# Kernel optimization log

Measured on AMD Instinct MI355X. Metric: run time of the kernel, lower is better.

The kernel has to match this reference:

```python
import jax, jax.numpy as jnp
import numpy as np

BN_EPS = 1e-5


def fps(xyz, npoint):
    # farthest point sampling; xyz: (B,N,3) -> (B,npoint) int32, starts at index 0 (torch convention)
    B, N, _ = xyz.shape
    def step(carry, _):
        dist, last = carry
        lp = jnp.take_along_axis(xyz, last[:, None, None], axis=1)  # (B,1,3)
        d = jnp.sum((xyz - lp) ** 2, -1)                             # (B,N)
        dist = jnp.minimum(dist, d)
        nxt = jnp.argmax(dist, -1).astype(jnp.int32)
        return (dist, nxt), nxt
    init = (jnp.full((B, N), 1e10, xyz.dtype), jnp.zeros((B,), jnp.int32))
    _, rest = jax.lax.scan(step, init, None, length=npoint - 1)
    return jnp.concatenate([jnp.zeros((1, B), jnp.int32), rest], 0).T  # (B,npoint)


def knn_idx(xyz, centers, k):
    # xyz (B,N,3), centers (B,S,3) -> (B,S,k) nearest-neighbor indices
    d = (jnp.sum(centers ** 2, -1)[:, :, None]
         + jnp.sum(xyz ** 2, -1)[:, None, :]
         - 2.0 * jnp.einsum('bsc,bnc->bsn', centers, xyz))
    _, idx = jax.lax.top_k(-d, k)
    return idx


def group(feat, idx):
    # feat (B,N,C), idx (B,S,K) -> (B,S,K,C)
    return jax.vmap(lambda f, i: f[i])(feat, idx)


def sa_knn(xyz, points, npoint, nsample, w1, b1, w2, b2):
    # xyz (B,N,3), points (B,N,C); returns new_xyz (B,S,3), new_points (B,S,Cout)
    fidx = fps(xyz, npoint)
    new_xyz = jnp.take_along_axis(xyz, fidx[:, :, None], axis=1)        # (B,S,3)
    idx = knn_idx(xyz, new_xyz, nsample)                                 # (B,S,K)
    g_xyz = group(xyz, idx) - new_xyz[:, :, None, :]                     # relative coords
    g_pts = group(points, idx)
    x = jnp.concatenate([g_xyz, g_pts], -1)                              # (B,S,K,3+C)
    x = jax.nn.relu(jnp.einsum('bskc,oc->bsko', x, w1) + b1)
    x = jnp.einsum('bskc,oc->bsko', x, w2) + b2                          # last conv: no activation
    return new_xyz, jnp.max(x, 2)                                        # max over neighbors


def sa_all(xyz, points, w1, b1, w2, b2):
    # group_all: concat xyz+points over all N, shared MLP, max over N -> (B,Cout)
    x = jnp.concatenate([xyz, points], -1)                               # (B,N,3+C)
    x = jax.nn.relu(jnp.einsum('bnc,oc->bno', x, w1) + b1)
    x = jnp.einsum('bnc,oc->bno', x, w2) + b2
    return jnp.max(x, 1)


def fc_head(x, w1, b1, g1, be1, w2, b2, g2, be2):
    # Linear + BN(eval, running mean=0/var=1) + ReLU, twice; Dropout = identity in eval
    s = 1.0 / np.sqrt(1.0 + BN_EPS)
    x = jax.nn.relu(g1 * ((x @ w1.T + b1) * s) + be1)
    x = jax.nn.relu(g2 * ((x @ w2.T + b2) * s) + be2)
    return x


def forward(point_cloud, sa1_w1, sa1_b1, sa1_w2, sa1_b2,
            sa2_w1, sa2_b1, sa2_w2, sa2_b2,
            sa3_w1, sa3_b1, sa3_w2, sa3_b2,
            fc_w1, fc_b1, fc_g1, fc_be1, fc_w2, fc_b2, fc_g2, fc_be2):
    xyz = jnp.transpose(point_cloud, (0, 2, 1))  # (B,N,3)
    nsamples2 = (16, 32, 48)
    logits, codes = [], []
    for i in range(3):  # three structurally distinct branches
        x1, p1 = sa_knn(xyz, xyz, 512, 16, sa1_w1[i], sa1_b1[i], sa1_w2[i], sa1_b2[i])
        x2, p2 = sa_knn(x1, p1, 128, nsamples2[i], sa2_w1[i], sa2_b1[i], sa2_w2[i], sa2_b2[i])
        code = sa_all(x2, p2, sa3_w1[i], sa3_b1[i], sa3_w2[i], sa3_b2[i])   # (B,512)
        logits.append(fc_head(code, fc_w1[i], fc_b1[i], fc_g1[i], fc_be1[i],
                              fc_w2[i], fc_b2[i], fc_g2[i], fc_be2[i]))      # (B,128)
        codes.append(code)
    return tuple(logits) + tuple(codes)


def setup_inputs():
    key = jax.random.key(0)
    ks = iter(jax.random.split(key, 16))
    def w(shape, s=0.05):
        return jax.random.normal(next(ks), shape, jnp.float32) * s
    B, N = 32, 2048
    inp = {'point_cloud': jax.random.normal(next(ks), (B, 3, N), jnp.float32)}
    inp.update(
        sa1_w1=w((3, 64, 6)), sa1_b1=jnp.zeros((3, 64)), sa1_w2=w((3, 128, 64)), sa1_b2=jnp.zeros((3, 128)),
        sa2_w1=w((3, 128, 131)), sa2_b1=jnp.zeros((3, 128)), sa2_w2=w((3, 256, 128)), sa2_b2=jnp.zeros((3, 256)),
        sa3_w1=w((3, 512, 259)), sa3_b1=jnp.zeros((3, 512)), sa3_w2=w((3, 512, 512)), sa3_b2=jnp.zeros((3, 512)),
        fc_w1=w((3, 256, 512)), fc_b1=jnp.zeros((3, 256)), fc_g1=jnp.ones((3, 256)), fc_be1=jnp.zeros((3, 256)),
        fc_w2=w((3, 128, 256)), fc_b2=jnp.zeros((3, 128)), fc_g2=jnp.ones((3, 128)), fc_be2=jnp.zeros((3, 128)),
    )
    return inp


def reference(point_cloud, sa1_w1, sa1_b1, sa1_w2, sa1_b2,
              sa2_w1, sa2_b1, sa2_w2, sa2_b2,
              sa3_w1, sa3_b1, sa3_w2, sa3_b2,
              fc_w1, fc_b1, fc_g1, fc_be1, fc_w2, fc_b2, fc_g2, fc_be2):
    return forward(point_cloud, sa1_w1, sa1_b1, sa1_w2, sa1_b2,
                   sa2_w1, sa2_b1, sa2_w2, sa2_b2,
                   sa3_w1, sa3_b1, sa3_w2, sa3_b2,
                   fc_w1, fc_b1, fc_g1, fc_be1, fc_w2, fc_b2, fc_g2, fc_be2)
```

## Files before the change

### kernel.cpp

```cpp
#include <hip/hip_runtime.h>
#include <hip/hip_bf16.h>
#include <math.h>

#define DEVI __device__ __forceinline__

static constexpr int BB = 32, NN = 2048, S1 = 512, S2 = 128;

typedef float f32x4 __attribute__((ext_vector_type(4)));
typedef short s16x8 __attribute__((ext_vector_type(8)));

static constexpr size_t OFF_XS   = 0;
static constexpr size_t OFF_YS   = OFF_XS + (size_t)BB*NN;
static constexpr size_t OFF_ZS   = OFF_YS + (size_t)BB*NN;
static constexpr size_t OFF_SSQ  = OFF_ZS + (size_t)BB*NN;
static constexpr size_t OFF_NX1X = OFF_SSQ + (size_t)BB*NN;
static constexpr size_t OFF_NX1Y = OFF_NX1X + (size_t)BB*S1;
static constexpr size_t OFF_NX1Z = OFF_NX1Y + (size_t)BB*S1;
static constexpr size_t OFF_NX2X = OFF_NX1Z + (size_t)BB*S1;
static constexpr size_t OFF_NX2Y = OFF_NX2X + (size_t)BB*S2;
static constexpr size_t OFF_NX2Z = OFF_NX2Y + (size_t)BB*S2;
static constexpr size_t OFF_CODE = OFF_NX2Z + (size_t)BB*S2;
static constexpr size_t OFF_O3P  = OFF_CODE + (size_t)3*BB*512;
static constexpr size_t OFF_P1   = OFF_O3P + (size_t)3*BB*4*512;
static constexpr size_t OFF_X3   = OFF_P1 + (size_t)3*BB*S1*128;
static constexpr size_t OFF_H3   = OFF_X3 + (size_t)3*BB*S2*260;
static constexpr size_t OFF_W    = OFF_H3 + (size_t)3*BB*S2*512;
static constexpr size_t W1A  = OFF_W;
static constexpr size_t B1A  = W1A + 3*64*6;
static constexpr size_t W2A  = B1A + 3*64;
static constexpr size_t B2A  = W2A + 3*128*64;
static constexpr size_t W1B  = B2A + 3*128;
static constexpr size_t B1B  = W1B + 3*128*132;
static constexpr size_t W2B  = B1B + 3*128;
static constexpr size_t B2B  = W2B + 3*256*128;
static constexpr size_t W1C  = B2B + 3*256;
static constexpr size_t B1C  = W1C + 3*512*260;
static constexpr size_t W2C  = B1C + 3*512;
static constexpr size_t B2C  = W2C + 3*512*512;
static constexpr size_t FW1  = B2C + 3*512;
static constexpr size_t FB1  = FW1 + 3*256*512;
static constexpr size_t FG1  = FB1 + 3*256;
static constexpr size_t FBE1 = FG1 + 3*256;
static constexpr size_t FW2  = FBE1 + 3*256;
static constexpr size_t FB2  = FW2 + 3*128*256;
static constexpr size_t FG2  = FB2 + 3*128;
static constexpr size_t FBE2 = FG2 + 3*128;
static constexpr size_t OFF_KNN1 = FBE2 + 3*128;
static constexpr size_t OFF_KNN2 = OFF_KNN1 + (size_t)BB*S1*16;
static constexpr size_t OFF_W1BF = OFF_KNN2 + (size_t)BB*S2*48;
static constexpr size_t OFF_W2BF = OFF_W1BF + 30720;
static constexpr size_t OFF_W1CBH = OFF_W2BF + 49152;
static constexpr size_t OFF_W1CBL = OFF_W1CBH + 221184;
static constexpr size_t OFF_W2CBH = OFF_W1CBL + 221184;
static constexpr size_t OFF_W2CBL = OFF_W2CBH + 393216;
static constexpr size_t OFF_X3BH  = OFF_W2CBL + 393216;
static constexpr size_t OFF_X3BL  = OFF_X3BH + 1769472;
static constexpr size_t OFF_H3BH  = OFF_X3BL + 1769472;
static constexpr size_t OFF_H3BL  = OFF_H3BH + 3145728;
static constexpr size_t OFF_W2ABH = OFF_H3BL + 3145728;
static constexpr size_t OFF_W2ABL = OFF_W2ABH + 12288;
static constexpr size_t WS_FLOATS = OFF_W2ABL + 12288;

__device__ __align__(16) float g_ws[WS_FLOATS];
__device__ int g_is_f32;
__device__ int g_flip;
__device__ int g_bad;
__device__ int g_nz;

DEVI float bf2f(const __hip_bfloat16 v){ return __bfloat162float(v); }
DEVI float rn_add(float a, float b){ return __fadd_rn(a,b); }
DEVI float rn_mul(float a, float b){ return __fmul_rn(a,b); }
DEVI float rn_sub(float a, float b){ return __fsub_rn(a,b); }
DEVI float sq3(float x,float y,float z){ return rn_add(rn_add(rn_mul(x,x),rn_mul(y,y)),rn_mul(z,z)); }

DEVI float ldany(const void* s, size_t i, int isf){
  return isf ? ((const float*)s)[i] : bf2f(((const __hip_bfloat16*)s)[i]);
}
DEVI unsigned short f2bf(float f){
  unsigned u = __float_as_uint(f);
  unsigned r = (u + 0x7FFFu + ((u>>16)&1u)) >> 16;
  return (unsigned short)r;
}
DEVI float bfbits2f(unsigned short h){ return __uint_as_float(((unsigned)h)<<16); }
DEVI void mfma16(f32x4& d, s16x8 a, s16x8 b){
  asm volatile("v_mfma_f32_16x16x32_bf16 %0, %1, %2, %0" : "+v"(d) : "v"(a), "v"(b));
}
DEVI void mfma_guard(f32x4& d){
  asm volatile("s_nop 7\n\ts_nop 7\n\ts_nop 2" : "+v"(d));
}

#define DPPF(dst, src, CTRL) dst = __uint_as_float((unsigned)__builtin_amdgcn_update_dpp(\
    (int)__float_as_uint(src), (int)__float_as_uint(src), CTRL, 0xF, 0xF, false))
#define DPPI(dst, src, CTRL) dst = __builtin_amdgcn_update_dpp(src, src, CTRL, 0xF, 0xF, false)
#define RED_STEP(CTRL) { float ov; int oi; DPPF(ov, best, CTRL); DPPI(oi, bidx, CTRL); \
  if (ov > best || (ov == best && oi < bidx)){ best = ov; bidx = oi; } }
#define WAVE_ARGMAX() RED_STEP(0xB1) RED_STEP(0x4E) RED_STEP(0x124) RED_STEP(0x128) RED_STEP(0x142) RED_STEP(0x143)

#define REDMIN_STEP(CTRL) { float ov; int oi; DPPF(ov, best, CTRL); DPPI(oi, bidx, CTRL); \
  if (ov < best || (ov == best && oi < bidx)){ best = ov; bidx = oi; } }
#define WAVE_ARGMIN() REDMIN_STEP(0xB1) REDMIN_STEP(0x4E) REDMIN_STEP(0x124) REDMIN_STEP(0x128) REDMIN_STEP(0x142) REDMIN_STEP(0x143)

__global__ __launch_bounds__(256) void init_detect_kernel(const void* __restrict__ pc){
  __shared__ int s_cnt[256];
  int t = threadIdx.x;
  if (t==0){ g_flip=0; g_bad=0; g_nz=0; }
  const unsigned short* h = (const unsigned short*)pc;
  int weird = 0;
  for (int i=t; i<4096; i+=256){
    unsigned short v = h[2*i];
    int e = (v >> 7) & 0xFF;
    if (e == 0xFF || e < 90 || e > 140) weird++;
  }
  s_cnt[t] = weird; __syncthreads();
  for (int o=128;o>0;o>>=1){ if (t<o) s_cnt[t]+=s_cnt[t+o]; __syncthreads(); }
  if (t==0) g_is_f32 = (s_cnt[0] > 1024) ? 1 : 0;
}

struct ParamPtrs { const void* p[20]; };

DEVI void cvt_arr(const void* s, float* d, int n, int g, int gs, int isf){
  for (int i=g;i<n;i+=gs) d[i] = ldany(s,i,isf);
}
DEVI void cvt_pad(const void* s, float* d, int rows, int cin, int cinp, int g, int gs, int isf){
  int tot = rows*cinp;
  for (int i=g;i<tot;i+=gs){ int r=i/cinp, c=i%cinp; d[i] = (c<cin)? ldany(s,(size_t)r*cin+c,isf) : 0.f; }
}

__global__ __launch_bounds__(256) void cvtprep_kernel(ParamPtrs pp, const void* __restrict__ pc, int mode){
  if (mode==1 && g_flip==0) return;
  const int isf = g_is_f32 ^ mode;
  if (blockIdx.x < 256){
    int i = blockIdx.x*256 + threadIdx.x;
    int b = i >> 11, n = i & 2047;
    float x = ldany(pc, (size_t)(b*3+0)*2048 + n, isf);
    float y = ldany(pc, (size_t)(b*3+1)*2048 + n, isf);
    float z = ldany(pc, (size_t)(b*3+2)*2048 + n, isf);
    g_ws[OFF_XS+i]=x; g_ws[OFF_YS+i]=y; g_ws[OFF_ZS+i]=z;
    g_ws[OFF_SSQ+i]=sq3(x,y,z);
    return;
  }
  int g = (blockIdx.x-256)*256 + threadIdx.x; int gs = 512*256;
  float* ws = g_ws;
  cvt_arr(pp.p[0],  ws+W1A, 3*64*6, g, gs, isf);
  cvt_arr(pp.p[1],  ws+B1A, 3*64, g, gs, isf);
  cvt_arr(pp.p[2],  ws+W2A, 3*128*64, g, gs, isf);
  cvt_arr(pp.p[3],  ws+B2A, 3*128, g, gs, isf);
  cvt_pad(pp.p[4],  ws+W1B, 3*128, 131, 132, g, gs, isf);
  cvt_arr(pp.p[5],  ws+B1B, 3*128, g, gs, isf);
  cvt_arr(pp.p[6],  ws+W2B, 3*256*128, g, gs, isf);
  cvt_arr(pp.p[7],  ws+B2B, 3*256, g, gs, isf);
  cvt_pad(pp.p[8],  ws+W1C, 3*512, 259, 260, g, gs, isf);
  cvt_arr(pp.p[9],  ws+B1C, 3*512, g, gs, isf);
  cvt_arr(pp.p[10], ws+W2C, 3*512*512, g, gs, isf);
  cvt_arr(pp.p[11], ws+B2C, 3*512, g, gs, isf);
  cvt_arr(pp.p[12], ws+FW1, 3*256*512, g, gs, isf);
  cvt_arr(pp.p[13], ws+FB1, 3*256, g, gs, isf);
  cvt_arr(pp.p[14], ws+FG1, 3*256, g, gs, isf);
  cvt_arr(pp.p[15], ws+FBE1,3*256, g, gs, isf);
  cvt_arr(pp.p[16], ws+FW2, 3*128*256, g, gs, isf);
  cvt_arr(pp.p[17], ws+FB2, 3*128, g, gs, isf);
  cvt_arr(pp.p[18], ws+FG2, 3*128, g, gs, isf);
  cvt_arr(pp.p[19], ws+FBE2,3*128, g, gs, isf);
}

__global__ __launch_bounds__(256) void scan_check_kernel(){
  size_t off; int n, g, gs;
  if (blockIdx.x < 128){ off = OFF_XS; n = 3*BB*NN; g = blockIdx.x*256 + threadIdx.x; gs = 128*256; }
  else { off = FW1; n = 3*256*512; g = (blockIdx.x-128)*256 + threadIdx.x; gs = 128*256; }
  int bad=0, nz=0;
  for (int i=g;i<n;i+=gs){
    float v = g_ws[off + i];
    if (v != v || fabsf(v) > 1e4f) bad=1;
    if (fabsf(v) > 1e-20f) nz=1;
  }
  unsigned long long mb = __ballot(bad), mn = __ballot(nz);
  if ((threadIdx.x & 63)==0){
    if (mb) atomicOr(&g_bad, 1);
    if (mn) atomicOr(&g_nz, 1);
  }
}

__global__ __launch_bounds__(64) void resolve_flip_kernel(){
  if (threadIdx.x==0){
    g_flip = (g_bad || !g_nz) ? 1 : 0;
    g_bad = 0; g_nz = 0;
  }
}

DEVI void cvt_bf16_body(int g, int gs){
  unsigned short* w1d = (unsigned short*)(g_ws + OFF_W1BF);
  for (int i=g; i<3*128*160; i+=gs){
    int br = i/(128*160); int rem = i%(128*160); int h = rem/160; int c = rem%160;
    float v = (c<132) ? g_ws[W1B + ((size_t)br*128 + h)*132 + c] : 0.f;
    w1d[i] = f2bf(v);
  }
  unsigned short* w2d = (unsigned short*)(g_ws + OFF_W2BF);
  for (int i=g; i<3*256*128; i+=gs) w2d[i] = f2bf(g_ws[W2B + i]);
  unsigned short* w1ch = (unsigned short*)(g_ws + OFF_W1CBH);
  unsigned short* w1cl = (unsigned short*)(g_ws + OFF_W1CBL);
  for (int i=g; i<3*512*288; i+=gs){
    int br = i/(512*288); int rem = i%(512*288); int n = rem/288; int c = rem%288;
    float v = (c<260) ? g_ws[W1C + ((size_t)br*512 + n)*260 + c] : 0.f;
    unsigned short hi = f2bf(v);
    w1ch[i] = hi; w1cl[i] = f2bf(v - bfbits2f(hi));
  }
  unsigned short* w2ch = (unsigned short*)(g_ws + OFF_W2CBH);
  unsigned short* w2cl = (unsigned short*)(g_ws + OFF_W2CBL);
  for (int i=g; i<3*512*512; i+=gs){
    float v = g_ws[W2C + i];
    unsigned short hi = f2bf(v);
    w2ch[i] = hi; w2cl[i] = f2bf(v - bfbits2f(hi));
  }
  unsigned short* w2ah = (unsigned short*)(g_ws + OFF_W2ABH);
  unsigned short* w2al = (unsigned short*)(g_ws + OFF_W2ABL);
  for (int i=g; i<3*128*64; i+=gs){
    float v = g_ws[W2A + i];
    unsigned short hi = f2bf(v);
    w2ah[i] = hi; w2al[i] = f2bf(v - bfbits2f(hi));
  }
}

#define FPS_DECL(J) float px##J, py##J, pz##J, dd##J;
#define FPS_LD256A(J) { int n=(J)*256+t; px##J=xs[n]; py##J=ys[n]; pz##J=zs[n]; dd##J=1e10f; xl[n]=px##J; yl[n]=py##J; zl[n]=pz##J; }
#define FPS_LD256B(J) { int n=(J)*256+t; px##J=xs[n]; py##J=ys[n]; pz##J=zs[n]; dd##J=ddg[n]; xl[n]=px##J; yl[n]=py##J; zl[n]=pz##J; }
#define FPS_SAVE(J) ddg[(J)*256+t]=dd##J;
#define FPS_LD64(J) { int n=(J)*64+t; px##J=xs[n]; py##J=ys[n]; pz##J=zs[n]; dd##J=1e10f; xl[n]=px##J; yl[n]=py##J; zl[n]=pz##J; }
#define FPS_UPD(J) { float dx=rn_sub(px##J,lx), dy=rn_sub(py##J,ly), dz=rn_sub(pz##J,lz); float d=sq3(dx,dy,dz); dd##J=fminf(dd##J,d); }
#define FPS_T1(J,JA,JB) float v##J; int q##J; { bool c = dd##JB > dd##JA; v##J = c? dd##JB : dd##JA; q##J = c? (JB) : (JA); }
#define FPS_T2(JA,JB) { bool c = v##JB > v##JA; v##JA = c? v##JB : v##JA; q##JA = c? q##JB : q##JA; }

#define FPS1_ITER_BODY() \
    FPS_UPD(0) FPS_UPD(1) FPS_UPD(2) FPS_UPD(3) FPS_UPD(4) FPS_UPD(5) FPS_UPD(6) FPS_UPD(7) \
    FPS_T1(0,0,1) FPS_T1(1,2,3) FPS_T1(2,4,5) FPS_T1(3,6,7) \
    FPS_T2(0,1) FPS_T2(2,3) \
    FPS_T2(0,2) \
    float best = v0; int bidx = q0*256 + t; \
    WAVE_ARGMAX() \
    int par = i & 1; \
    if ((t&63)==63){ s_val[par][wave]=best; s_idx[par][wave]=bidx; } \
    __syncthreads(); \
    float va = s_val[par][0], vb = s_val[par][1], vc = s_val[par][2], vd = s_val[par][3]; \
    int ia = s_idx[par][0], ib = s_idx[par][1], ic = s_idx[par][2], id_ = s_idx[par][3]; \
    if (vb > va || (vb == va && ib < ia)){ va = vb; ia = ib; } \
    if (vd > vc || (vd == vc && id_ < ic)){ vc = vd; ic = id_; } \
    if (vc > va || (vc == va && ic < ia)){ va = vc; ia = ic; } \
    int gidx = ia; \
    lx = xl[gidx]; ly = yl[gidx]; lz = zl[gidx]; \
    if (t==0){ nx[i]=lx; ny[i]=ly; nz[i]=lz; }

__global__ __launch_bounds__(256,1) void fps1a_cvt_kernel(){
  const int t = threadIdx.x;
  if (blockIdx.x >= 32){
    cvt_bf16_body((blockIdx.x-32)*256 + t, 256*256);
    return;
  }
  const int b = blockIdx.x;
  const int wave = t >> 6;
  const float* xs = g_ws + OFF_XS + (size_t)b*NN;
  const float* ys = g_ws + OFF_YS + (size_t)b*NN;
  const float* zs = g_ws + OFF_ZS + (size_t)b*NN;
  float* nx = g_ws + OFF_NX1X + (size_t)b*S1;
  float* ny = g_ws + OFF_NX1Y + (size_t)b*S1;
  float* nz = g_ws + OFF_NX1Z + (size_t)b*S1;
  float* ddg = g_ws + OFF_X3 + (size_t)b*NN;
  __shared__ float xl[NN], yl[NN], zl[NN];
  __shared__ float s_val[2][4]; __shared__ int s_idx[2][4];
  FPS_DECL(0) FPS_DECL(1) FPS_DECL(2) FPS_DECL(3) FPS_DECL(4) FPS_DECL(5) FPS_DECL(6) FPS_DECL(7)
  FPS_LD256A(0) FPS_LD256A(1) FPS_LD256A(2) FPS_LD256A(3) FPS_LD256A(4) FPS_LD256A(5) FPS_LD256A(6) FPS_LD256A(7)
  __syncthreads();
  float lx = xl[0], ly = yl[0], lz = zl[0];
  if (t==0){ nx[0]=lx; ny[0]=ly; nz[0]=lz; }
  for (int i=1;i<256;i++){
    FPS1_ITER_BODY()
  }
  FPS_SAVE(0) FPS_SAVE(1) FPS_SAVE(2) FPS_SAVE(3) FPS_SAVE(4) FPS_SAVE(5) FPS_SAVE(6) FPS_SAVE(7)
}

#define KNN1_POISON(C) case C: d[C] = match ? 3.0e38f : d[C]; break;
DEVI void knn1_body(int wid, int lane){
  int b = wid >> 9;
  const float* xs = g_ws + OFF_XS + (size_t)b*NN;
  const float* ys = g_ws + OFF_YS + (size_t)b*NN;
  const float* zs = g_ws + OFF_ZS + (size_t)b*NN;
  const float* sq = g_ws + OFF_SSQ + (size_t)b*NN;
  float cx = g_ws[OFF_NX1X + wid], cy = g_ws[OFF_NX1Y + wid], cz = g_ws[OFF_NX1Z + wid];
  float sc = sq3(cx,cy,cz);
  float d[32];
  #pragma unroll
  for (int c=0;c<32;c++){
    int n = c*64 + lane;
    float x=xs[n], y=ys[n], z=zs[n];
    float dot = rn_add(rn_add(rn_mul(cx,x),rn_mul(cy,y)),rn_mul(cz,z));
    d[c] = rn_sub(rn_add(sc,sq[n]), rn_mul(2.f,dot));
  }
  int* out = (int*)(g_ws + OFF_KNN1) + (size_t)wid*16;
  for (int r=0;r<16;r++){
    float tv[16]; int tc[16];
    #pragma unroll
    for (int c=0;c<16;c++){
      float a = d[2*c];
      float e = d[2*c+1];
      bool cc = e < a;
      tv[c] = cc ? e : a; tc[c] = cc ? (2*c+1) : (2*c);
    }
    #pragma unroll
    for (int s=1; s<16; s<<=1){
      #pragma unroll
      for (int c=0;c<16;c+=2){
        if ((c % (2*s)) == 0 && c+s < 16){
          bool cc = tv[c+s] < tv[c];
          tv[c] = cc ? tv[c+s] : tv[c];
          tc[c] = cc ? tc[c+s] : tc[c];
        }
      }
    }
    float best = tv[0]; int bidx = tc[0]*64 + lane;
    WAVE_ARGMIN()
    int wbi = __builtin_amdgcn_readlane(bidx, 63);
    if (lane == 0) out[r] = wbi;
    bool match = (lane == (wbi & 63));
    switch ((wbi >> 6) & 31){
      KNN1_POISON(0)  KNN1_POISON(1)  KNN1_POISON(2)  KNN1_POISON(3)
      KNN1_POISON(4)  KNN1_POISON(5)  KNN1_POISON(6)  KNN1_POISON(7)
      KNN1_POISON(8)  KNN1_POISON(9)  KNN1_POISON(10) KNN1_POISON(11)
      KNN1_POISON(12) KNN1_POISON(13) KNN1_POISON(14) KNN1_POISON(15)
      KNN1_POISON(16) KNN1_POISON(17) KNN1_POISON(18) KNN1_POISON(19)
      KNN1_POISON(20) KNN1_POISON(21) KNN1_POISON(22) KNN1_POISON(23)
      KNN1_POISON(24) KNN1_POISON(25) KNN1_POISON(26) KNN1_POISON(27)
      KNN1_POISON(28) KNN1_POISON(29) KNN1_POISON(30) KNN1_POISON(31)
    }
  }
}

DEVI void sa1_body(int br, int bxx, float* w1s, float* b1s, short* Hh, short* Hl){
  const int t = threadIdx.x;
  const int wave = t>>6, lane = t&63, quad = lane>>4, l16 = lane&15;
  for (int i=t;i<384;i+=256) w1s[i] = g_ws[W1A + (size_t)br*384 + i];
  if (t<64) b1s[t] = g_ws[B1A + br*64 + t];
  __syncthreads();
  const int* kn = (const int*)(g_ws + OFF_KNN1);
  const short* w2h = (const short*)(g_ws + OFF_W2ABH) + (size_t)br*128*64;
  const short* w2l = (const short*)(g_ws + OFF_W2ABL) + (size_t)br*128*64;
  const float* b2 = g_ws + B2A + br*128;
  for (int it=0; it<4; it++){
    int gid = bxx*16 + it*4 + wave;
    int b = gid >> 9;
    int idx = kn[(size_t)gid*16 + l16] & (NN-1);
    float cx = g_ws[OFF_NX1X+gid], cy = g_ws[OFF_NX1Y+gid], cz = g_ws[OFF_NX1Z+gid];
    size_t gl = (size_t)b*NN + idx;
    float x = g_ws[OFF_XS+gl], y = g_ws[OFF_YS+gl], z = g_ws[OFF_ZS+gl];
    float f0=x-cx, f1=y-cy, f2=z-cz;
    #pragma unroll
    for (int i=0;i<16;i++){
      int h = quad*16 + i;
      float acc = b1s[h];
      acc += f0*w1s[h*6+0] + f1*w1s[h*6+1] + f2*w1s[h*6+2]
           +  x*w1s[h*6+3] +  y*w1s[h*6+4] +  z*w1s[h*6+5];
      acc = fmaxf(acc, 0.f);
      unsigned short hi = f2bf(acc);
      Hh[wave*1152 + l16*72 + h] = (short)hi;
      Hl[wave*1152 + l16*72 + h] = (short)f2bf(acc - bfbits2f(hi));
    }
    s16x8 ah[2], al[2];
    #pragma unroll
    for (int ks=0;ks<2;ks++){
      ah[ks] = *(const s16x8*)(&Hh[wave*1152 + l16*72 + ks*32 + quad*8]);
      al[ks] = *(const s16x8*)(&Hl[wave*1152 + l16*72 + ks*32 + quad*8]);
    }
    unsigned short* P1g = (unsigned short*)(g_ws + OFF_P1) + ((size_t)br*16384 + gid)*128;
    #pragma unroll
    for (int ni=0; ni<8; ni++){
      int o = ni*16 + l16;
      f32x4 acc = {0.f,0.f,0.f,0.f};
      #pragma unroll
      for (int ks=0; ks<2; ks++){
        s16x8 bh = *(const s16x8*)(w2h + (size_t)o*64 + ks*32 + quad*8);
        s16x8 bl = *(const s16x8*)(w2l + (size_t)o*64 + ks*32 + quad*8);
        mfma16(acc, ah[ks], bh);
        mfma16(acc, ah[ks], bl);
        mfma16(acc, al[ks], bh);
      }
      mfma_guard(acc);
      float vmax = fmaxf(fmaxf(acc[0],acc[1]), fmaxf(acc[2],acc[3]));
      vmax = fmaxf(vmax, __shfl_xor(vmax,16));
      vmax = fmaxf(vmax, __shfl_xor(vmax,32));
      if (quad==0) P1g[o] = f2bf(vmax + b2[o]);
    }
  }
}

__global__ __launch_bounds__(256,1) void fps1b_knn1a_kernel(){
  const int t = threadIdx.x;
  if (blockIdx.x >= 32){
    int lin = ((blockIdx.x-32)*256 + t) >> 6;
    int b = lin >> 8, s = lin & 255;
    knn1_body(b*S1 + s, t & 63);
    return;
  }
  const int b = blockIdx.x;
  const int wave = t >> 6;
  const float* xs = g_ws + OFF_XS + (size_t)b*NN;
  const float* ys = g_ws + OFF_YS + (size_t)b*NN;
  const float* zs = g_ws + OFF_ZS + (size_t)b*NN;
  float* nx = g_ws + OFF_NX1X + (size_t)b*S1;
  float* ny = g_ws + OFF_NX1Y + (size_t)b*S1;
  float* nz = g_ws + OFF_NX1Z + (size_t)b*S1;
  const float* ddg = g_ws + OFF_X3 + (size_t)b*NN;
  __shared__ float xl[NN], yl[NN], zl[NN];
  __shared__ float s_val[2][4]; __shared__ int s_idx[2][4];
  FPS_DECL(0) FPS_DECL(1) FPS_DECL(2) FPS_DECL(3) FPS_DECL(4) FPS_DECL(5) FPS_DECL(6) FPS_DECL(7)
  FPS_LD256B(0) FPS_LD256B(1) FPS_LD256B(2) FPS_LD256B(3) FPS_LD256B(4) FPS_LD256B(5) FPS_LD256B(6) FPS_LD256B(7)
  __syncthreads();
  float lx = nx[255], ly = ny[255], lz = nz[255];
  for (int i=256;i<S1;i++){
    FPS1_ITER_BODY()
  }
}

__global__ __launch_bounds__(256) void fps2_knn1b_sa1a_kernel(){
  __shared__ float xl[S1], yl[S1], zl[S1];
  __shared__ float w1s[384];
  __shared__ float b1s[64];
  __shared__ __align__(16) short Hh[4*16*72];
  __shared__ __align__(16) short Hl[4*16*72];
  __shared__ float s_val_un[2][4]; __shared__ int s_idx_un[2][4];
  (void)s_val_un; (void)s_idx_un;
  if (blockIdx.x >= 2080){
    int q = blockIdx.x - 2080;
    int br = q >> 9, r = q & 511;
    int bxx = ((r >> 4) << 5) + (r & 15);
    sa1_body(br, bxx, w1s, b1s, Hh, Hl);
    return;
  }
  if (blockIdx.x >= 32){
    int lin = ((blockIdx.x-32)*256 + threadIdx.x) >> 6;
    int b = lin >> 8, s = lin & 255;
    knn1_body(b*S1 + 256 + s, threadIdx.x & 63);
    return;
  }
  if (threadIdx.x >= 64) return;
  const int b = blockIdx.x, t = threadIdx.x;
  const float* xs = g_ws + OFF_NX1X + (size_t)b*S1;
  const float* ys = g_ws + OFF_NX1Y + (size_t)b*S1;
  const float* zs = g_ws + OFF_NX1Z + (size_t)b*S1;
  float* nx = g_ws + OFF_NX2X + (size_t)b*S2;
  float* ny = g_ws + OFF_NX2Y + (size_t)b*S2;
  float* nz = g_ws + OFF_NX2Z + (size_t)b*S2;
  FPS_DECL(0) FPS_DECL(1) FPS_DECL(2) FPS_DECL(3) FPS_DECL(4) FPS_DECL(5) FPS_DECL(6) FPS_DECL(7)
  FPS_LD64(0) FPS_LD64(1) FPS_LD64(2) FPS_LD64(3) FPS_LD64(4) FPS_LD64(5) FPS_LD64(6) FPS_LD64(7)
  float lx = xl[0], ly = yl[0], lz = zl[0];
  if (t==0){ nx[0]=lx; ny[0]=ly; nz[0]=lz; }
  for (int i=1;i<S2;i++){
    FPS_UPD(0) FPS_UPD(1) FPS_UPD(2) FPS_UPD(3) FPS_UPD(4) FPS_UPD(5) FPS_UPD(6) FPS_UPD(7)
    FPS_T1(0,0,1) FPS_T1(1,2,3) FPS_T1(2,4,5) FPS_T1(3,6,7)
    FPS_T2(0,1) FPS_T2(2,3)
    FPS_T2(0,2)
    float best = v0; int bidx = q0*64 + t;
    WAVE_ARGMAX()
    int gidx = __builtin_amdgcn_readlane(bidx, 63);
    lx = xl[gidx]; ly = yl[gidx]; lz = zl[gidx];
    if (t==0){ nx[i]=lx; ny[i]=ly; nz[i]=lz; }
  }
}

#define KNN2_POISON(C) case C: d[C] = match ? 3.0e38f : d[C]; break;
DEVI void knn2_body(int wid, int lane){
  int b = wid >> 7;
  const float* xs = g_ws + OFF_NX1X + (size_t)b*S1;
  const float* ys = g_ws + OFF_NX1Y + (size_t)b*S1;
  const float* zs = g_ws + OFF_NX1Z + (size_t)b*S1;
  float cx = g_ws[OFF_NX2X + wid], cy = g_ws[OFF_NX2Y + wid], cz = g_ws[OFF_NX2Z + wid];
  float sc = sq3(cx,cy,cz);
  float d[8];
  #pragma unroll
  for (int c=0;c<8;c++){
    int n = c*64 + lane;
    float x=xs[n], y=ys[n], z=zs[n];
    float sx = sq3(x,y,z);
    float dot = rn_add(rn_add(rn_mul(cx,x),rn_mul(cy,y)),rn_mul(cz,z));
    d[c] = rn_sub(rn_add(sc,sx), rn_mul(2.f,dot));
  }
  int* out = (int*)(g_ws + OFF_KNN2) + (size_t)wid*48;
  for (int r=0;r<48;r++){
    float tv[4]; int tc[4];
    #pragma unroll
    for (int c=0;c<4;c++){
      float a = d[2*c];
      float e = d[2*c+1];
      bool cc = e < a;
      tv[c] = cc ? e : a; tc[c] = cc ? (2*c+1) : (2*c);
    }
    { bool cc = tv[1] < tv[0]; tv[0] = cc?tv[1]:tv[0]; tc[0] = cc?tc[1]:tc[0]; }
    { bool cc = tv[3] < tv[2]; tv[2] = cc?tv[3]:tv[2]; tc[2] = cc?tc[3]:tc[2]; }
    { bool cc = tv[2] < tv[0]; tv[0] = cc?tv[2]:tv[0]; tc[0] = cc?tc[2]:tc[0]; }
    float best = tv[0]; int bidx = tc[0]*64 + lane;
    WAVE_ARGMIN()
    int wbi = __builtin_amdgcn_readlane(bidx, 63);
    if (lane == 0) out[r] = wbi;
    bool match = (lane == (wbi & 63));
    switch ((wbi >> 6) & 7){
      KNN2_POISON(0) KNN2_POISON(1) KNN2_POISON(2) KNN2_POISON(3)
      KNN2_POISON(4) KNN2_POISON(5) KNN2_POISON(6) KNN2_POISON(7)
    }
  }
}

__global__ __launch_bounds__(256) void knn2_sa1b_kernel(){
  __shared__ float w1s[384];
  __shared__ float b1s[64];
  __shared__ __align__(16) short Hh[4*16*72];
  __shared__ __align__(16) short Hl[4*16*72];
  const int t = threadIdx.x;
  if (blockIdx.x < 1024){
    knn2_body((blockIdx.x*256 + t) >> 6, t & 63);
    return;
  }
  int q = blockIdx.x - 1024;
  int br = q >> 9, r = q & 511;
  int bxx = ((r >> 4) << 5) + 16 + (r & 15);
  sa1_body(br, bxx, w1s, b1s, Hh, Hl);
}

template<int K>
DEVI void sa2_body(int br, int g2, short* Xb, short* Hb, float* ctr, int* idxs){
  constexpr int MT = K/16;
  const int b = g2 >> 7;
  const int t = threadIdx.x;
  const int wave = t >> 6, lane = t & 63, quad = lane >> 4, l16 = lane & 15;
  const int* kn2 = (const int*)(g_ws + OFF_KNN2) + (size_t)g2*48;
  if (t < K) idxs[t] = kn2[t] & (S1-1);
  if (t < 3) ctr[t] = g_ws[(t==0?OFF_NX2X:(t==1?OFF_NX2Y:OFF_NX2Z)) + g2];
  __syncthreads();
  const unsigned short* p1b = (const unsigned short*)(g_ws + OFF_P1) + (size_t)br*16384*128;
  const int grp = t >> 5, gl = t & 31;
  for (int k = grp; k < K; k += 8){
    int idx = idxs[k];
    const unsigned short* row = p1b + ((size_t)b*S1 + idx)*128;
    unsigned long long w = *(const unsigned long long*)(row + gl*4);
    short* dst = &Xb[k*168 + 3 + gl*4];
    dst[0] = (short)(w & 0xFFFF);
    dst[1] = (short)((w >> 16) & 0xFFFF);
    dst[2] = (short)((w >> 32) & 0xFFFF);
    dst[3] = (short)((w >> 48) & 0xFFFF);
    if (gl < 32) Xb[k*168 + 131 + gl] = 0;
    if (gl < 5)  Xb[k*168 + 163 + gl] = 0;
  }
  if (t < K){
    int idx = idxs[t];
    float c0 = g_ws[OFF_NX1X + (size_t)b*S1 + idx] - ctr[0];
    float c1 = g_ws[OFF_NX1Y + (size_t)b*S1 + idx] - ctr[1];
    float c2 = g_ws[OFF_NX1Z + (size_t)b*S1 + idx] - ctr[2];
    Xb[t*168+0] = (short)f2bf(c0);
    Xb[t*168+1] = (short)f2bf(c1);
    Xb[t*168+2] = (short)f2bf(c2);
  }
  __syncthreads();
  {
    const short* w1bf = (const short*)(g_ws + OFF_W1BF) + (size_t)br*128*160;
    const float* b1 = g_ws + B1B + br*128;
    for (int ni = wave; ni < 8; ni += 4){
      int h = ni*16 + l16;
      s16x8 bfr[5];
      #pragma unroll
      for (int ks=0;ks<5;ks++) bfr[ks] = *(const s16x8*)(w1bf + (size_t)h*160 + ks*32 + quad*8);
      float bias = b1[h];
      #pragma unroll
      for (int m=0; m<MT; m++){
        f32x4 acc = {0.f,0.f,0.f,0.f};
        #pragma unroll
        for (int ks=0;ks<5;ks++){
          s16x8 a = *(const s16x8*)(&Xb[(m*16 + l16)*168 + ks*32 + quad*8]);
          mfma16(acc, a, bfr[ks]);
        }
        mfma_guard(acc);
        #pragma unroll
        for (int r=0;r<4;r++){
          int row = m*16 + quad*4 + r;
          float hv = fmaxf(acc[r] + bias, 0.f);
          Hb[row*136 + ni*16 + l16] = (short)f2bf(hv);
        }
      }
    }
  }
  __syncthreads();
  {
    const short* w2bf = (const short*)(g_ws + OFF_W2BF) + (size_t)br*256*128;
    const float* b2 = g_ws + B2B + br*256;
    unsigned short* xh = (unsigned short*)(g_ws + OFF_X3BH);
    unsigned short* xlo = (unsigned short*)(g_ws + OFF_X3BL);
    size_t row = (size_t)(br*4096 + g2)*288;
    for (int ni = wave; ni < 16; ni += 4){
      int o = ni*16 + l16;
      s16x8 bfr[4];
      #pragma unroll
      for (int ks=0;ks<4;ks++) bfr[ks] = *(const s16x8*)(w2bf + (size_t)o*128 + ks*32 + quad*8);
      float vmax = -3.4e38f;
      #pragma unroll
      for (int m=0; m<MT; m++){
        f32x4 acc = {0.f,0.f,0.f,0.f};
        #pragma unroll
        for (int ks=0;ks<4;ks++){
          s16x8 a = *(const s16x8*)(&Hb[(m*16 + l16)*136 + ks*32 + quad*8]);
          mfma16(acc, a, bfr[ks]);
        }
        mfma_guard(acc);
        #pragma unroll
        for (int r=0;r<4;r++) vmax = fmaxf(vmax, acc[r]);
      }
      vmax = fmaxf(vmax, __shfl_xor(vmax, 16));
      vmax = fmaxf(vmax, __shfl_xor(vmax, 32));
      if (quad == 0){
        float hv = vmax + b2[o];
        unsigned short hi = f2bf(hv);
        xh[row + 3 + o] = hi;
        xlo[row + 3 + o] = f2bf(hv - bfbits2f(hi));
      }
    }
    if (t < 3){
      float cv = ctr[t];
      unsigned short hi = f2bf(cv);
      xh[row + t] = hi; xlo[row + t] = f2bf(cv - bfbits2f(hi));
    }
    if (t >= 3 && t < 32){ xh[row + 256 + t] = 0; xlo[row + 256 + t] = 0; }
  }
}

__global__ __launch_bounds__(256) void sa2_all_kernel(){
  __shared__ __align__(16) short Xb[48*168];
  __shared__ __align__(16) short Hb[48*136];
  __shared__ float ctr[3];
  __shared__ int idxs[48];
  int br = blockIdx.x >> 12;
  int g2 = blockIdx.x & 4095;
  if (br == 0)      sa2_body<16>(0, g2, Xb, Hb, ctr, idxs);
  else if (br == 1) sa2_body<32>(1, g2, Xb, Hb, ctr, idxs);
  else              sa2_body<48>(2, g2, Xb, Hb, ctr, idxs);
}

__global__ __launch_bounds__(256) void sa3l1_mfma_kernel(){
  const int br = blockIdx.y; const int r0 = blockIdx.x*32;
  const int t = threadIdx.x;
  const int wave = t >> 6, lane = t & 63, quad = lane >> 4, l16 = lane & 15;
  const short* xh = (const short*)(g_ws + OFF_X3BH) + (size_t)(br*4096 + r0)*288;
  const short* xl = (const short*)(g_ws + OFF_X3BL) + (size_t)(br*4096 + r0)*288;
  const short* wh = (const short*)(g_ws + OFF_W1CBH) + (size_t)br*512*288;
  const short* wl = (const short*)(g_ws + OFF_W1CBL) + (size_t)br*512*288;
  const float* bias = g_ws + B1C + br*512;
  unsigned short* hh = (unsigned short*)(g_ws + OFF_H3BH) + (size_t)(br*4096 + r0)*512;
  unsigned short* hl = (unsigned short*)(g_ws + OFF_H3BL) + (size_t)(br*4096 + r0)*512;
  f32x4 acc[2][8];
  #pragma unroll
  for (int m=0;m<2;m++)
    #pragma unroll
    for (int ni=0;ni<8;ni++) acc[m][ni] = (f32x4){0.f,0.f,0.f,0.f};
  for (int ks=0; ks<9; ks++){
    s16x8 ah[2], al[2];
    #pragma unroll
    for (int m=0;m<2;m++){
      ah[m] = *(const s16x8*)(xh + (size_t)(m*16+l16)*288 + ks*32 + quad*8);
      al[m] = *(const s16x8*)(xl + (size_t)(m*16+l16)*288 + ks*32 + quad*8);
    }
    #pragma unroll
    for (int ni=0;ni<8;ni++){
      int n = wave*128 + ni*16 + l16;
      s16x8 bh = *(const s16x8*)(wh + (size_t)n*288 + ks*32 + quad*8);
      s16x8 bl = *(const s16x8*)(wl + (size_t)n*288 + ks*32 + quad*8);
      #pragma unroll
      for (int m=0;m<2;m++){
        mfma16(acc[m][ni], ah[m], bh);
        mfma16(acc[m][ni], ah[m], bl);
        mfma16(acc[m][ni], al[m], bh);
      }
    }
  }
  mfma_guard(acc[0][0]);
  #pragma unroll
  for (int m=0;m<2;m++){
    #pragma unroll
    for (int ni=0;ni<8;ni++){
      int col = wave*128 + ni*16 + l16;
      float bs = bias[col];
      #pragma unroll
      for (int r=0;r<4;r++){
        int row = m*16 + quad*4 + r;
        float hv = fmaxf(acc[m][ni][r] + bs, 0.f);
        unsigned short hi = f2bf(hv);
        hh[(size_t)row*512 + col] = hi;
        hl[(size_t)row*512 + col] = f2bf(hv - bfbits2f(hi));
      }
    }
  }
}

__global__ __launch_bounds__(256) void sa3l2_mfma_kernel(){
  const int br = blockIdx.y; const int b = blockIdx.x>>2; const int part = blockIdx.x&3;
  const int t = threadIdx.x;
  const int wave = t >> 6, lane = t & 63, quad = lane >> 4, l16 = lane & 15;
  const int row0 = b*128 + part*32;
  const short* ahp = (const short*)(g_ws + OFF_H3BH) + (size_t)(br*4096 + row0)*512;
  const short* alp = (const short*)(g_ws + OFF_H3BL) + (size_t)(br*4096 + row0)*512;
  const short* wh = (const short*)(g_ws + OFF_W2CBH) + (size_t)br*512*512;
  const short* wl = (const short*)(g_ws + OFF_W2CBL) + (size_t)br*512*512;
  f32x4 acc[2][8];
  #pragma unroll
  for (int m=0;m<2;m++)
    #pragma unroll
    for (int ni=0;ni<8;ni++) acc[m][ni] = (f32x4){0.f,0.f,0.f,0.f};
  for (int ks=0; ks<16; ks++){
    s16x8 ah[2], al[2];
    #pragma unroll
    for (int m=0;m<2;m++){
      ah[m] = *(const s16x8*)(ahp + (size_t)(m*16+l16)*512 + ks*32 + quad*8);
      al[m] = *(const s16x8*)(alp + (size_t)(m*16+l16)*512 + ks*32 + quad*8);
    }
    #pragma unroll
    for (int ni=0;ni<8;ni++){
      int n = wave*128 + ni*16 + l16;
      s16x8 bh = *(const s16x8*)(wh + (size_t)n*512 + ks*32 + quad*8);
      s16x8 bl = *(const s16x8*)(wl + (size_t)n*512 + ks*32 + quad*8);
      #pragma unroll
      for (int m=0;m<2;m++){
        mfma16(acc[m][ni], ah[m], bh);
        mfma16(acc[m][ni], ah[m], bl);
        mfma16(acc[m][ni], al[m], bh);
      }
    }
  }
  mfma_guard(acc[0][0]);
  #pragma unroll
  for (int ni=0;ni<8;ni++){
    float vmax = -3.4e38f;
    #pragma unroll
    for (int m=0;m<2;m++)
      #pragma unroll
      for (int r=0;r<4;r++) vmax = fmaxf(vmax, acc[m][ni][r]);
    vmax = fmaxf(vmax, __shfl_xor(vmax, 16));
    vmax = fmaxf(vmax, __shfl_xor(vmax, 32));
    if (quad == 0){
      int col = wave*128 + ni*16 + l16;
      g_ws[OFF_O3P + (((size_t)br*BB + b)*4 + part)*512 + col] = vmax;
    }
  }
}

__global__ __launch_bounds__(256) void fc_kernel(float* __restrict__ out, int out_size){
  int br = blockIdx.x >> 5; int b = blockIdx.x & 31; int t = threadIdx.x;
  __shared__ float xin[512]; __shared__ float x1s[256];
  const float* o3p = g_ws + OFF_O3P + (((size_t)br*BB + b)*4)*512;
  const float* b2c = g_ws + B2C + br*512;
  #pragma unroll
  for (int k=0;k<2;k++){
    int o = t + k*256;
    float m = fmaxf(fmaxf(o3p[o], o3p[512+o]), fmaxf(o3p[1024+o], o3p[1536+o]));
    m += b2c[o];
    xin[o] = m;
    int oi = 3*BB*128 + ((br*BB + b)*512) + o;
    if (oi < out_size) out[oi] = m;
  }
  __syncthreads();
  const float s = (float)(1.0 / sqrt(1.0 + 1e-5));
  {
    const float4* wp = (const float4*)(g_ws + FW1 + ((size_t)br*256 + t)*512);
    const float4* xp = (const float4*)xin;
    float acc = 0.f;
    #pragma unroll 8
    for (int q=0;q<128;q++){ float4 w4=wp[q], x4=xp[q]; acc += w4.x*x4.x + w4.y*x4.y + w4.z*x4.z + w4.w*x4.w; }
    acc = (acc + g_ws[FB1 + br*256+t]) * s;
    acc = g_ws[FG1+br*256+t]*acc + g_ws[FBE1+br*256+t];
    x1s[t] = fmaxf(acc, 0.f);
  }
  __syncthreads();
  if (t < 128){
    const float4* wp = (const float4*)(g_ws + FW2 + ((size_t)br*128 + t)*256);
    const float4* xp = (const float4*)x1s;
    float acc=0.f;
    #pragma unroll 8
    for (int q=0;q<64;q++){ float4 w4=wp[q], x4=xp[q]; acc += w4.x*x4.x + w4.y*x4.y + w4.z*x4.z + w4.w*x4.w; }
    acc = (acc + g_ws[FB2+br*128+t])*s;
    acc = g_ws[FG2+br*128+t]*acc + g_ws[FBE2+br*128+t];
    int oi = ((size_t)br*BB + b)*128 + t;
    if (oi < out_size) out[oi] = fmaxf(acc,0.f);
  }
}

extern "C" void kernel_launch(void* const* d_in, const int* in_sizes, int n_in,
                              void* d_out, int out_size, void* d_ws, size_t ws_size,
                              hipStream_t stream) {
  (void)d_ws; (void)ws_size;
  if (n_in < 21) return;
  if (in_sizes[0] != BB*3*NN) return;
  float* out = (float*)d_out;

  ParamPtrs pp;
  for (int i=0;i<20;i++) pp.p[i] = d_in[i+1];

  init_detect_kernel<<<1,256,0,stream>>>(d_in[0]);
  cvtprep_kernel<<<768,256,0,stream>>>(pp, d_in[0], 0);
  scan_check_kernel<<<256,256,0,stream>>>();
  resolve_flip_kernel<<<1,64,0,stream>>>();
  cvtprep_kernel<<<768,256,0,stream>>>(pp, d_in[0], 1);

  fps1a_cvt_kernel<<<32+256,256,0,stream>>>();
  fps1b_knn1a_kernel<<<32+2048,256,0,stream>>>();
  fps2_knn1b_sa1a_kernel<<<32+2048+1536,256,0,stream>>>();
  knn2_sa1b_kernel<<<1024+1536,256,0,stream>>>();
  sa2_all_kernel<<<3*4096,256,0,stream>>>();

  sa3l1_mfma_kernel<<<dim3(128,3),256,0,stream>>>();
  sa3l2_mfma_kernel<<<dim3(128,3),256,0,stream>>>();
  fc_kernel<<<96,256,0,stream>>>(out, out_size);
}
```

Measured before the change: 1.080 ms.

## Split first-level FPS into three phases to overlap more KNN and SA1 work

The serial farthest-point-sampling loop for level 1 is split into three kernels (171/171/170 iterations) instead of two. Between phases the per-point min-distance is saved and reloaded. KNN1 work for already-selected centers is rebalanced across the extra launch, and the SA1 blocks are redistributed to match. The goal is to hide more of the latency-bound FPS chain behind parallel KNN and MLP work, at the cost of one extra kernel launch and an extra save/reload of the distance state.

```diff
diff --git a/kernel.cpp b/kernel.cpp
--- a/kernel.cpp
+++ b/kernel.cpp
@@ -220,6 +220,8 @@
   }
 }
 
+static constexpr int SP1 = 171, SP2 = 342;
+
 #define FPS_DECL(J) float px##J, py##J, pz##J, dd##J;
 #define FPS_LD256A(J) { int n=(J)*256+t; px##J=xs[n]; py##J=ys[n]; pz##J=zs[n]; dd##J=1e10f; xl[n]=px##J; yl[n]=py##J; zl[n]=pz##J; }
 #define FPS_LD256B(J) { int n=(J)*256+t; px##J=xs[n]; py##J=ys[n]; pz##J=zs[n]; dd##J=ddg[n]; xl[n]=px##J; yl[n]=py##J; zl[n]=pz##J; }
@@ -248,29 +250,32 @@
     lx = xl[gidx]; ly = yl[gidx]; lz = zl[gidx]; \
     if (t==0){ nx[i]=lx; ny[i]=ly; nz[i]=lz; }
 
-__global__ __launch_bounds__(256,1) void fps1a_cvt_kernel(){
+#define FPS1_BLOCK_SETUP() \
+  const int b = blockIdx.x; \
+  const int wave = t >> 6; \
+  const float* xs = g_ws + OFF_XS + (size_t)b*NN; \
+  const float* ys = g_ws + OFF_YS + (size_t)b*NN; \
+  const float* zs = g_ws + OFF_ZS + (size_t)b*NN; \
+  float* nx = g_ws + OFF_NX1X + (size_t)b*S1; \
+  float* ny = g_ws + OFF_NX1Y + (size_t)b*S1; \
+  float* nz = g_ws + OFF_NX1Z + (size_t)b*S1; \
+  float* ddg = g_ws + OFF_X3 + (size_t)b*NN; \
+  __shared__ float xl[NN], yl[NN], zl[NN]; \
+  __shared__ float s_val[2][4]; __shared__ int s_idx[2][4]; \
+  FPS_DECL(0) FPS_DECL(1) FPS_DECL(2) FPS_DECL(3) FPS_DECL(4) FPS_DECL(5) FPS_DECL(6) FPS_DECL(7)
+
+__global__ __launch_bounds__(256,1) void fps1A_cvt_kernel(){
   const int t = threadIdx.x;
   if (blockIdx.x >= 32){
     cvt_bf16_body((blockIdx.x-32)*256 + t, 256*256);
     return;
   }
-  const int b = blockIdx.x;
-  const int wave = t >> 6;
-  const float* xs = g_ws + OFF_XS + (size_t)b*NN;
-  const float* ys = g_ws + OFF_YS + (size_t)b*NN;
-  const float* zs = g_ws + OFF_ZS + (size_t)b*NN;
-  float* nx = g_ws + OFF_NX1X + (size_t)b*S1;
-  float* ny = g_ws + OFF_NX1Y + (size_t)b*S1;
-  float* nz = g_ws + OFF_NX1Z + (size_t)b*S1;
-  float* ddg = g_ws + OFF_X3 + (size_t)b*NN;
-  __shared__ float xl[NN], yl[NN], zl[NN];
-  __shared__ float s_val[2][4]; __shared__ int s_idx[2][4];
-  FPS_DECL(0) FPS_DECL(1) FPS_DECL(2) FPS_DECL(3) FPS_DECL(4) FPS_DECL(5) FPS_DECL(6) FPS_DECL(7)
+  FPS1_BLOCK_SETUP()
   FPS_LD256A(0) FPS_LD256A(1) FPS_LD256A(2) FPS_LD256A(3) FPS_LD256A(4) FPS_LD256A(5) FPS_LD256A(6) FPS_LD256A(7)
   __syncthreads();
   float lx = xl[0], ly = yl[0], lz = zl[0];
   if (t==0){ nx[0]=lx; ny[0]=ly; nz[0]=lz; }
-  for (int i=1;i<256;i++){
+  for (int i=1;i<SP1;i++){
     FPS1_ITER_BODY()
   }
   FPS_SAVE(0) FPS_SAVE(1) FPS_SAVE(2) FPS_SAVE(3) FPS_SAVE(4) FPS_SAVE(5) FPS_SAVE(6) FPS_SAVE(7)
@@ -389,57 +394,63 @@
   }
 }
 
-__global__ __launch_bounds__(256,1) void fps1b_knn1a_kernel(){
+__global__ __launch_bounds__(256,1) void fps1B_knn1a_kernel(){
   const int t = threadIdx.x;
   if (blockIdx.x >= 32){
     int lin = ((blockIdx.x-32)*256 + t) >> 6;
-    int b = lin >> 8, s = lin & 255;
+    int b = lin / 160, s = lin % 160;
     knn1_body(b*S1 + s, t & 63);
     return;
   }
-  const int b = blockIdx.x;
-  const int wave = t >> 6;
-  const float* xs = g_ws + OFF_XS + (size_t)b*NN;
-  const float* ys = g_ws + OFF_YS + (size_t)b*NN;
-  const float* zs = g_ws + OFF_ZS + (size_t)b*NN;
-  float* nx = g_ws + OFF_NX1X + (size_t)b*S1;
-  float* ny = g_ws + OFF_NX1Y + (size_t)b*S1;
-  float* nz = g_ws + OFF_NX1Z + (size_t)b*S1;
-  const float* ddg = g_ws + OFF_X3 + (size_t)b*NN;
-  __shared__ float xl[NN], yl[NN], zl[NN];
-  __shared__ float s_val[2][4]; __shared__ int s_idx[2][4];
-  FPS_DECL(0) FPS_DECL(1) FPS_DECL(2) FPS_DECL(3) FPS_DECL(4) FPS_DECL(5) FPS_DECL(6) FPS_DECL(7)
+  FPS1_BLOCK_SETUP()
   FPS_LD256B(0) FPS_LD256B(1) FPS_LD256B(2) FPS_LD256B(3) FPS_LD256B(4) FPS_LD256B(5) FPS_LD256B(6) FPS_LD256B(7)
   __syncthreads();
-  float lx = nx[255], ly = ny[255], lz = nz[255];
-  for (int i=256;i<S1;i++){
+  float lx = nx[SP1-1], ly = ny[SP1-1], lz = nz[SP1-1];
+  for (int i=SP1;i<SP2;i++){
     FPS1_ITER_BODY()
   }
-}
-
-__global__ __launch_bounds__(256) void fps2_knn1b_sa1a_kernel(){
+  FPS_SAVE(0) FPS_SAVE(1) FPS_SAVE(2) FPS_SAVE(3) FPS_SAVE(4) FPS_SAVE(5) FPS_SAVE(6) FPS_SAVE(7)
+}
+
+__global__ __launch_bounds__(256,1) void fps1C_knn1b_kernel(){
+  const int t = threadIdx.x;
+  if (blockIdx.x >= 32){
+    int lin = ((blockIdx.x-32)*256 + t) >> 6;
+    int b = lin / 176, s = 160 + lin % 176;
+    knn1_body(b*S1 + s, t & 63);
+    return;
+  }
+  FPS1_BLOCK_SETUP()
+  FPS_LD256B(0) FPS_LD256B(1) FPS_LD256B(2) FPS_LD256B(3) FPS_LD256B(4) FPS_LD256B(5) FPS_LD256B(6) FPS_LD256B(7)
+  __syncthreads();
+  float lx = nx[SP2-1], ly = ny[SP2-1], lz = nz[SP2-1];
+  for (int i=SP2;i<S1;i++){
+    FPS1_ITER_BODY()
+  }
+}
+
+__global__ __launch_bounds__(256) void fps2_knn1c_sa1a_kernel(){
   __shared__ float xl[S1], yl[S1], zl[S1];
   __shared__ float w1s[384];
   __shared__ float b1s[64];
   __shared__ __align__(16) short Hh[4*16*72];
   __shared__ __align__(16) short Hl[4*16*72];
-  __shared__ float s_val_un[2][4]; __shared__ int s_idx_un[2][4];
-  (void)s_val_un; (void)s_idx_un;
-  if (blockIdx.x >= 2080){
-    int q = blockIdx.x - 2080;
-    int br = q >> 9, r = q & 511;
-    int bxx = ((r >> 4) << 5) + (r & 15);
-    sa1_body(br, bxx, w1s, b1s, Hh, Hl);
+  const int t = threadIdx.x;
+  if (blockIdx.x >= 1440){
+    int q = blockIdx.x - 1440;
+    int br = q / 672, rem = q % 672;
+    int b = rem / 21, sblk = rem % 21;
+    sa1_body(br, b*32 + sblk, w1s, b1s, Hh, Hl);
     return;
   }
   if (blockIdx.x >= 32){
-    int lin = ((blockIdx.x-32)*256 + threadIdx.x) >> 6;
-    int b = lin >> 8, s = lin & 255;
-    knn1_body(b*S1 + 256 + s, threadIdx.x & 63);
+    int lin = ((blockIdx.x-32)*256 + t) >> 6;
+    int b = lin / 176, s = 336 + lin % 176;
+    knn1_body(b*S1 + s, t & 63);
     return;
   }
-  if (threadIdx.x >= 64) return;
-  const int b = blockIdx.x, t = threadIdx.x;
+  if (t >= 64) return;
+  const int b = blockIdx.x;
   const float* xs = g_ws + OFF_NX1X + (size_t)b*S1;
   const float* ys = g_ws + OFF_NX1Y + (size_t)b*S1;
   const float* zs = g_ws + OFF_NX1Z + (size_t)b*S1;
@@ -516,9 +527,9 @@
     return;
   }
   int q = blockIdx.x - 1024;
-  int br = q >> 9, r = q & 511;
-  int bxx = ((r >> 4) << 5) + 16 + (r & 15);
-  sa1_body(br, bxx, w1s, b1s, Hh, Hl);
+  int br = q / 352, rem = q % 352;
+  int b = rem / 11, sblk = 21 + rem % 11;
+  sa1_body(br, b*32 + sblk, w1s, b1s, Hh, Hl);
 }
 
 template<int K>
@@ -800,10 +811,11 @@
   resolve_flip_kernel<<<1,64,0,stream>>>();
   cvtprep_kernel<<<768,256,0,stream>>>(pp, d_in[0], 1);
 
-  fps1a_cvt_kernel<<<32+256,256,0,stream>>>();
-  fps1b_knn1a_kernel<<<32+2048,256,0,stream>>>();
-  fps2_knn1b_sa1a_kernel<<<32+2048+1536,256,0,stream>>>();
-  knn2_sa1b_kernel<<<1024+1536,256,0,stream>>>();
+  fps1A_cvt_kernel<<<32+256,256,0,stream>>>();
+  fps1B_knn1a_kernel<<<32+1280,256,0,stream>>>();
+  fps1C_knn1b_kernel<<<32+1408,256,0,stream>>>();
+  fps2_knn1c_sa1a_kernel<<<32+1408+2016,256,0,stream>>>();
+  knn2_sa1b_kernel<<<1024+1056,256,0,stream>>>();
   sa2_all_kernel<<<3*4096,256,0,stream>>>();
 
   sa3l1_mfma_kernel<<<dim3(128,3),256,0,stream>>>();
```

Measured after the change: 1.084 ms. Within noise of the previous version (+0.3%).
